# Kernel tuning notes

Hardware: AMD Instinct MI355X
Metric: run time of the kernel (lower is better)

Reference implementation:

```python
import jax, jax.numpy as jnp
import numpy as np

EPS_DEFAULT = 1.1920928955078125e-07  # torch fp32 finfo eps used when eps=None


def rms_norm(x, ndims, weight=None, eps=EPS_DEFAULT):
    # normalize over the last `ndims` dims, matching F.rms_norm semantics
    axes = tuple(range(x.ndim - ndims, x.ndim))
    ms = jnp.mean(jnp.square(x), axis=axes, keepdims=True)
    out = x * jax.lax.rsqrt(ms + eps)
    if weight is not None:
        out = out * weight  # weight broadcasts over trailing dims
    return out


def setup_inputs() -> dict:
    key = jax.random.key(0)
    ks = jax.random.split(key, 9)
    B, S = 32, 512
    return {
        "x": jax.random.normal(ks[0], (B, S, 12, 24), dtype=jnp.float32),
        "y": jax.random.normal(ks[1], (B, S, 12, 16), dtype=jnp.float32),
        "z": jax.random.normal(ks[2], (B, S, 12, 16, 24), dtype=jnp.float32),
        "w0": jax.random.uniform(ks[3], (24,), dtype=jnp.float32),
        "w1": jax.random.uniform(ks[4], (12, 16), dtype=jnp.float32),
        "w2": jax.random.uniform(ks[5], (24,), dtype=jnp.float32),
        "w3": jax.random.uniform(ks[6], (24,), dtype=jnp.float32),
        "w4": jax.random.uniform(ks[7], (12, 16), dtype=jnp.float32),
        "w5": jax.random.uniform(ks[8], (24,), dtype=jnp.float32),
    }


def reference(x, y, z, w0, w1, w2, w3, w4, w5):
    # x branch: norm over (24,), then (12,24), then (24,)
    x = rms_norm(x, 1, w0)
    x = rms_norm(x, 2, None)
    x = rms_norm(x, 1, w3)
    # y branch: norm over (16,) eps=1e-3, then (12,16) twice
    y = rms_norm(y, 1, None, eps=0.001)
    y = rms_norm(y, 2, w1)
    y = rms_norm(y, 2, w4)
    # z branch: norm over (24,), then (12,16,24) eps=1e-2, then (24,)
    z = rms_norm(z, 1, w2)
    z = rms_norm(z, 3, None, eps=0.01)
    z = rms_norm(z, 1, w5)
    return (x, y, z)
```

## Files before the change

### kernel.cpp

```cpp
#include <hip/hip_runtime.h>

#define EPS_DEF 1.1920928955078125e-07f

typedef float f4 __attribute__((ext_vector_type(4)));


__launch_bounds__(192)
__global__ void fused_rms_kernel(const float* __restrict__ x,
                                 const float* __restrict__ y,
                                 const float* __restrict__ z,
                                 const float* __restrict__ w0,
                                 const float* __restrict__ w1,
                                 const float* __restrict__ w2,
                                 const float* __restrict__ w3,
                                 const float* __restrict__ w4,
                                 const float* __restrict__ w5,
                                 float* __restrict__ ox,
                                 float* __restrict__ oy,
                                 float* __restrict__ oz)
{
    __shared__ __align__(16) float2 part[1152];
    __shared__ __align__(16) float  xs[288];
    __shared__ __align__(16) float  ys[192];
    __shared__ float2 rw[192];
    __shared__ float2 rwx[12];
    __shared__ float  rwy[12];
    __shared__ __align__(16) float w0sqs[24], w03s[24];
    __shared__ __align__(16) float w1sqs[192], w14s[192];
    __shared__ float wpart[3][4];

    const int tid = threadIdx.x;
    const int bid = blockIdx.x;
    const int j6  = tid % 6;
    const int c4  = j6 * 4;
    const int r0  = tid / 6;

    float w2v[4], w5v[4];
    #pragma unroll
    for (int k = 0; k < 4; ++k) { w2v[k] = w2[c4 + k]; w5v[k] = w5[c4 + k]; }

    const f4* zp = (const f4*)(z + (size_t)bid * 4608);
    f4 zr[6];
    #pragma unroll
    for (int i = 0; i < 6; ++i) zr[i] = zp[tid + 192 * i];

    if (tid < 72) {
        ((f4*)xs)[tid] = ((const f4*)(x + (size_t)bid * 288))[tid];
    } else if (tid < 120) {
        int t = tid - 72;
        ((f4*)ys)[t] = ((const f4*)(y + (size_t)bid * 192))[t];
    } else if (tid < 144) {
        int q = tid - 120;
        float a0 = w0[q], a3 = w3[q];
        w0sqs[q] = a0 * a0; w03s[q] = a0 * a3;
    }
    {
        float a1 = w1[tid], a4 = w4[tid];
        w1sqs[tid] = a1 * a1;
        w14s[tid]  = a1 * a4;
    }

    #pragma unroll
    for (int i = 0; i < 6; ++i) {
        f4 q = zr[i];
        float s0 = q.x * q.x;
        s0 = fmaf(q.y, q.y, s0); s0 = fmaf(q.z, q.z, s0); s0 = fmaf(q.w, q.w, s0);
        float t0 = q.x * w2v[0], t1 = q.y * w2v[1], t2 = q.z * w2v[2], t3 = q.w * w2v[3];
        float sw = t0 * t0;
        sw = fmaf(t1, t1, sw); sw = fmaf(t2, t2, sw); sw = fmaf(t3, t3, sw);
        part[tid + 192 * i] = make_float2(s0, sw);
    }
    __syncthreads();

    float s0 = 0.f, swz = 0.f;
    {
        const f4* pr = (const f4*)&part[6 * tid];
        #pragma unroll
        for (int k = 0; k < 3; ++k) {
            f4 p = pr[k];
            s0  += p.x + p.z;
            swz += p.y + p.w;
        }
    }
    const float r1 = rsqrtf(s0 * (1.f / 24.f) + EPS_DEF);
    rw[tid] = make_float2(r1, swz);
    float p0 = r1 * r1 * swz, p1 = 0.f, p2 = 0.f, p3 = 0.f;

    if (tid < 12) {
        const float* row = &xs[tid * 24];
        float a0 = 0.f, aw = 0.f;
        #pragma unroll
        for (int j = 0; j < 24; ++j) {
            float v = row[j];
            a0 = fmaf(v, v, a0);
            aw = fmaf(v * v, w0sqs[j], aw);
        }
        float r1x = rsqrtf(a0 * (1.f / 24.f) + EPS_DEF);
        rwx[tid] = make_float2(r1x, aw);
        p1 = r1x * r1x * aw;
    } else if (tid < 24) {
        int i = tid - 12;
        const float* row = &ys[i * 16];
        const float* wq  = &w1sqs[i * 16];
        float a0 = 0.f, aw = 0.f;
        #pragma unroll
        for (int j = 0; j < 16; ++j) {
            float v = row[j];
            a0 = fmaf(v, v, a0);
            aw = fmaf(v * v, wq[j], aw);
        }
        float r1y = rsqrtf(a0 * (1.f / 16.f) + 1e-3f);
        rwy[i] = r1y;
        p2 = r1y * r1y * a0;
        p3 = r1y * r1y * aw;
    }

    #pragma unroll
    for (int d = 32; d; d >>= 1) {
        p0 += __shfl_down(p0, d, 64);
        p1 += __shfl_down(p1, d, 64);
        p2 += __shfl_down(p2, d, 64);
        p3 += __shfl_down(p3, d, 64);
    }
    if ((tid & 63) == 0) {
        int w = tid >> 6;
        wpart[w][0] = p0; wpart[w][1] = p1; wpart[w][2] = p2; wpart[w][3] = p3;
    }
    __syncthreads();

    const float Sz  = wpart[0][0] + wpart[1][0] + wpart[2][0];
    const float Sx  = wpart[0][1] + wpart[1][1] + wpart[2][1];
    const float Sy0 = wpart[0][2] + wpart[1][2] + wpart[2][2];
    const float Sy1 = wpart[0][3] + wpart[1][3] + wpart[2][3];

    const float cZ  = rsqrtf(Sz  * (1.f / 4608.f) + 0.01f);
    const float cX  = rsqrtf(Sx  * (1.f / 288.f)  + EPS_DEF);
    const float c2y = rsqrtf(Sy0 * (1.f / 192.f)  + EPS_DEF);
    const float c3y = rsqrtf(c2y * c2y * Sy1 * (1.f / 192.f) + EPS_DEF);
    const float cZsq = cZ * cZ;

    {
        float w25r[4];
        #pragma unroll
        for (int k = 0; k < 4; ++k) w25r[k] = w2v[k] * w5v[k];
        f4* ozp = (f4*)(oz + (size_t)bid * 4608);
        #pragma unroll
        for (int i = 0; i < 6; ++i) {
            float2 rr = rw[r0 + 32 * i];
            float r3 = rsqrtf(cZsq * rr.x * rr.x * rr.y * (1.f / 24.f) + EPS_DEF);
            float a  = rr.x * cZ * r3;
            f4 q = zr[i];
            q.x *= a * w25r[0];
            q.y *= a * w25r[1];
            q.z *= a * w25r[2];
            q.w *= a * w25r[3];
            __builtin_nontemporal_store(q, ozp + tid + 192 * i);
        }
    }

    if (tid < 72) {
        int row = tid / 6;
        float2 rr = rwx[row];
        float r3 = rsqrtf(cX * cX * rr.x * rr.x * rr.y * (1.f / 24.f) + EPS_DEF);
        float ax = rr.x * cX * r3;
        f4 q = ((const f4*)xs)[tid];
        f4 wf = ((const f4*)w03s)[tid % 6];
        q.x *= ax * wf.x;
        q.y *= ax * wf.y;
        q.z *= ax * wf.z;
        q.w *= ax * wf.w;
        __builtin_nontemporal_store(q, (f4*)(ox + (size_t)bid * 288) + tid);
    } else if (tid < 120) {
        int t = tid - 72;
        float ay = rwy[t / 4] * c2y * c3y;
        f4 q = ((const f4*)ys)[t];
        f4 wf = ((const f4*)w14s)[t];
        q.x *= ay * wf.x;
        q.y *= ay * wf.y;
        q.z *= ay * wf.z;
        q.w *= ay * wf.w;
        __builtin_nontemporal_store(q, (f4*)(oy + (size_t)bid * 192) + t);
    }
}

extern "C" void kernel_launch(void* const* d_in, const int* in_sizes, int n_in,
                              void* d_out, int out_size, void* d_ws, size_t ws_size,
                              hipStream_t stream) {
    const float* x  = (const float*)d_in[0];
    const float* y  = (const float*)d_in[1];
    const float* z  = (const float*)d_in[2];
    const float* w0 = (const float*)d_in[3];
    const float* w1 = (const float*)d_in[4];
    const float* w2 = (const float*)d_in[5];
    const float* w3 = (const float*)d_in[6];
    const float* w4 = (const float*)d_in[7];
    const float* w5 = (const float*)d_in[8];

    float* out = (float*)d_out;
    const size_t NX = (size_t)32 * 512 * 12 * 24;
    const size_t NY = (size_t)32 * 512 * 12 * 16;
    float* ox = out;
    float* oy = out + NX;
    float* oz = out + NX + NY;

    const int nblk = 32 * 512;
    hipLaunchKernelGGL(fused_rms_kernel, dim3(nblk), dim3(192), 0, stream,
                       x, y, z, w0, w1, w2, w3, w4, w5, ox, oy, oz);
}
```

Baseline: 123.3 us.

## Process two sequence slots per block and use nontemporal loads

Each 192-thread block now handles two (b,s) slots instead of one, halving the grid and loading both slots' z/x/y data up front so more memory loads are in flight per thread. The weight-product setup and barriers are amortized over two slots, and the wave reductions carry eight partial sums instead of four. Input loads are switched to nontemporal. The cost is double the register and LDS footprint per block, which may reduce occupancy.

Result: no change. 122.2 us (-0.9%).

```diff
diff --git a/kernel.cpp b/kernel.cpp
--- a/kernel.cpp
+++ b/kernel.cpp
@@ -19,18 +19,18 @@
                                  float* __restrict__ oy,
                                  float* __restrict__ oz)
 {
-    __shared__ __align__(16) float2 part[1152];
-    __shared__ __align__(16) float  xs[288];
-    __shared__ __align__(16) float  ys[192];
-    __shared__ float2 rw[192];
-    __shared__ float2 rwx[12];
-    __shared__ float  rwy[12];
+    __shared__ __align__(16) float2 part[2][1152];
+    __shared__ __align__(16) float  xs[2][288];
+    __shared__ __align__(16) float  ys[2][192];
+    __shared__ float2 rw[2][192];
+    __shared__ float2 rwx[2][12];
+    __shared__ float  rwy[2][12];
     __shared__ __align__(16) float w0sqs[24], w03s[24];
     __shared__ __align__(16) float w1sqs[192], w14s[192];
-    __shared__ float wpart[3][4];
+    __shared__ float wpart[3][8];
 
     const int tid = threadIdx.x;
-    const int bid = blockIdx.x;
+    const size_t slA = (size_t)blockIdx.x * 2;
     const int j6  = tid % 6;
     const int c4  = j6 * 4;
     const int r0  = tid / 6;
@@ -39,16 +39,26 @@
     #pragma unroll
     for (int k = 0; k < 4; ++k) { w2v[k] = w2[c4 + k]; w5v[k] = w5[c4 + k]; }
 
-    const f4* zp = (const f4*)(z + (size_t)bid * 4608);
-    f4 zr[6];
-    #pragma unroll
-    for (int i = 0; i < 6; ++i) zr[i] = zp[tid + 192 * i];
+    f4 zr[2][6];
+    #pragma unroll
+    for (int s = 0; s < 2; ++s) {
+        const f4* zp = (const f4*)(z + (slA + s) * 4608);
+        #pragma unroll
+        for (int i = 0; i < 6; ++i)
+            zr[s][i] = __builtin_nontemporal_load(zp + tid + 192 * i);
+    }
 
     if (tid < 72) {
-        ((f4*)xs)[tid] = ((const f4*)(x + (size_t)bid * 288))[tid];
+        #pragma unroll
+        for (int s = 0; s < 2; ++s)
+            ((f4*)xs[s])[tid] =
+                __builtin_nontemporal_load((const f4*)(x + (slA + s) * 288) + tid);
     } else if (tid < 120) {
         int t = tid - 72;
-        ((f4*)ys)[t] = ((const f4*)(y + (size_t)bid * 192))[t];
+        #pragma unroll
+        for (int s = 0; s < 2; ++s)
+            ((f4*)ys[s])[t] =
+                __builtin_nontemporal_load((const f4*)(y + (slA + s) * 192) + t);
     } else if (tid < 144) {
         int q = tid - 120;
         float a0 = w0[q], a3 = w3[q];
@@ -61,125 +71,140 @@
     }
 
     #pragma unroll
-    for (int i = 0; i < 6; ++i) {
-        f4 q = zr[i];
-        float s0 = q.x * q.x;
-        s0 = fmaf(q.y, q.y, s0); s0 = fmaf(q.z, q.z, s0); s0 = fmaf(q.w, q.w, s0);
-        float t0 = q.x * w2v[0], t1 = q.y * w2v[1], t2 = q.z * w2v[2], t3 = q.w * w2v[3];
-        float sw = t0 * t0;
-        sw = fmaf(t1, t1, sw); sw = fmaf(t2, t2, sw); sw = fmaf(t3, t3, sw);
-        part[tid + 192 * i] = make_float2(s0, sw);
+    for (int s = 0; s < 2; ++s) {
+        #pragma unroll
+        for (int i = 0; i < 6; ++i) {
+            f4 q = zr[s][i];
+            float a0 = q.x * q.x;
+            a0 = fmaf(q.y, q.y, a0); a0 = fmaf(q.z, q.z, a0); a0 = fmaf(q.w, q.w, a0);
+            float t0 = q.x * w2v[0], t1 = q.y * w2v[1], t2 = q.z * w2v[2], t3 = q.w * w2v[3];
+            float aw = t0 * t0;
+            aw = fmaf(t1, t1, aw); aw = fmaf(t2, t2, aw); aw = fmaf(t3, t3, aw);
+            part[s][tid + 192 * i] = make_float2(a0, aw);
+        }
     }
     __syncthreads();
 
-    float s0 = 0.f, swz = 0.f;
-    {
-        const f4* pr = (const f4*)&part[6 * tid];
+    float p[8];
+    #pragma unroll
+    for (int q = 0; q < 8; ++q) p[q] = 0.f;
+
+    #pragma unroll
+    for (int s = 0; s < 2; ++s) {
+        float a0 = 0.f, aw = 0.f;
+        const f4* pr = (const f4*)&part[s][6 * tid];
         #pragma unroll
         for (int k = 0; k < 3; ++k) {
-            f4 p = pr[k];
-            s0  += p.x + p.z;
-            swz += p.y + p.w;
-        }
-    }
-    const float r1 = rsqrtf(s0 * (1.f / 24.f) + EPS_DEF);
-    rw[tid] = make_float2(r1, swz);
-    float p0 = r1 * r1 * swz, p1 = 0.f, p2 = 0.f, p3 = 0.f;
+            f4 pp = pr[k];
+            a0 += pp.x + pp.z;
+            aw += pp.y + pp.w;
+        }
+        float r1 = rsqrtf(a0 * (1.f / 24.f) + EPS_DEF);
+        rw[s][tid] = make_float2(r1, aw);
+        p[4 * s + 0] = r1 * r1 * aw;
+    }
 
     if (tid < 12) {
-        const float* row = &xs[tid * 24];
-        float a0 = 0.f, aw = 0.f;
-        #pragma unroll
-        for (int j = 0; j < 24; ++j) {
-            float v = row[j];
-            a0 = fmaf(v, v, a0);
-            aw = fmaf(v * v, w0sqs[j], aw);
-        }
-        float r1x = rsqrtf(a0 * (1.f / 24.f) + EPS_DEF);
-        rwx[tid] = make_float2(r1x, aw);
-        p1 = r1x * r1x * aw;
+        #pragma unroll
+        for (int s = 0; s < 2; ++s) {
+            const float* row = &xs[s][tid * 24];
+            float a0 = 0.f, aw = 0.f;
+            #pragma unroll
+            for (int j = 0; j < 24; ++j) {
+                float v = row[j];
+                a0 = fmaf(v, v, a0);
+                aw = fmaf(v * v, w0sqs[j], aw);
+            }
+            float r1x = rsqrtf(a0 * (1.f / 24.f) + EPS_DEF);
+            rwx[s][tid] = make_float2(r1x, aw);
+            p[4 * s + 1] = r1x * r1x * aw;
+        }
     } else if (tid < 24) {
         int i = tid - 12;
-        const float* row = &ys[i * 16];
-        const float* wq  = &w1sqs[i * 16];
-        float a0 = 0.f, aw = 0.f;
-        #pragma unroll
-        for (int j = 0; j < 16; ++j) {
-            float v = row[j];
-            a0 = fmaf(v, v, a0);
-            aw = fmaf(v * v, wq[j], aw);
-        }
-        float r1y = rsqrtf(a0 * (1.f / 16.f) + 1e-3f);
-        rwy[i] = r1y;
-        p2 = r1y * r1y * a0;
-        p3 = r1y * r1y * aw;
+        #pragma unroll
+        for (int s = 0; s < 2; ++s) {
+            const float* row = &ys[s][i * 16];
+            const float* wq  = &w1sqs[i * 16];
+            float a0 = 0.f, aw = 0.f;
+            #pragma unroll
+            for (int j = 0; j < 16; ++j) {
+                float v = row[j];
+                a0 = fmaf(v, v, a0);
+                aw = fmaf(v * v, wq[j], aw);
+            }
+            float r1y = rsqrtf(a0 * (1.f / 16.f) + 1e-3f);
+            rwy[s][i] = r1y;
+            p[4 * s + 2] = r1y * r1y * a0;
+            p[4 * s + 3] = r1y * r1y * aw;
+        }
     }
 
     #pragma unroll
     for (int d = 32; d; d >>= 1) {
-        p0 += __shfl_down(p0, d, 64);
-        p1 += __shfl_down(p1, d, 64);
-        p2 += __shfl_down(p2, d, 64);
-        p3 += __shfl_down(p3, d, 64);
+        #pragma unroll
+        for (int q = 0; q < 8; ++q) p[q] += __shfl_down(p[q], d, 64);
     }
     if ((tid & 63) == 0) {
         int w = tid >> 6;
-        wpart[w][0] = p0; wpart[w][1] = p1; wpart[w][2] = p2; wpart[w][3] = p3;
+        #pragma unroll
+        for (int q = 0; q < 8; ++q) wpart[w][q] = p[q];
     }
     __syncthreads();
 
-    const float Sz  = wpart[0][0] + wpart[1][0] + wpart[2][0];
-    const float Sx  = wpart[0][1] + wpart[1][1] + wpart[2][1];
-    const float Sy0 = wpart[0][2] + wpart[1][2] + wpart[2][2];
-    const float Sy1 = wpart[0][3] + wpart[1][3] + wpart[2][3];
-
-    const float cZ  = rsqrtf(Sz  * (1.f / 4608.f) + 0.01f);
-    const float cX  = rsqrtf(Sx  * (1.f / 288.f)  + EPS_DEF);
-    const float c2y = rsqrtf(Sy0 * (1.f / 192.f)  + EPS_DEF);
-    const float c3y = rsqrtf(c2y * c2y * Sy1 * (1.f / 192.f) + EPS_DEF);
-    const float cZsq = cZ * cZ;
-
-    {
-        float w25r[4];
-        #pragma unroll
-        for (int k = 0; k < 4; ++k) w25r[k] = w2v[k] * w5v[k];
-        f4* ozp = (f4*)(oz + (size_t)bid * 4608);
+    float w25r[4];
+    #pragma unroll
+    for (int k = 0; k < 4; ++k) w25r[k] = w2v[k] * w5v[k];
+
+    #pragma unroll
+    for (int s = 0; s < 2; ++s) {
+        const float Sz  = wpart[0][4*s+0] + wpart[1][4*s+0] + wpart[2][4*s+0];
+        const float Sx  = wpart[0][4*s+1] + wpart[1][4*s+1] + wpart[2][4*s+1];
+        const float Sy0 = wpart[0][4*s+2] + wpart[1][4*s+2] + wpart[2][4*s+2];
+        const float Sy1 = wpart[0][4*s+3] + wpart[1][4*s+3] + wpart[2][4*s+3];
+
+        const float cZ  = rsqrtf(Sz  * (1.f / 4608.f) + 0.01f);
+        const float cX  = rsqrtf(Sx  * (1.f / 288.f)  + EPS_DEF);
+        const float c2y = rsqrtf(Sy0 * (1.f / 192.f)  + EPS_DEF);
+        const float c3y = rsqrtf(c2y * c2y * Sy1 * (1.f / 192.f) + EPS_DEF);
+        const float cZsq = cZ * cZ;
+
+        f4* ozp = (f4*)(oz + (slA + s) * 4608);
         #pragma unroll
         for (int i = 0; i < 6; ++i) {
-            float2 rr = rw[r0 + 32 * i];
+            float2 rr = rw[s][r0 + 32 * i];
             float r3 = rsqrtf(cZsq * rr.x * rr.x * rr.y * (1.f / 24.f) + EPS_DEF);
             float a  = rr.x * cZ * r3;
-            f4 q = zr[i];
+            f4 q = zr[s][i];
             q.x *= a * w25r[0];
             q.y *= a * w25r[1];
             q.z *= a * w25r[2];
             q.w *= a * w25r[3];
             __builtin_nontemporal_store(q, ozp + tid + 192 * i);
         }
-    }
-
-    if (tid < 72) {
-        int row = tid / 6;
-        float2 rr = rwx[row];
-        float r3 = rsqrtf(cX * cX * rr.x * rr.x * rr.y * (1.f / 24.f) + EPS_DEF);
-        float ax = rr.x * cX * r3;
-        f4 q = ((const f4*)xs)[tid];
-        f4 wf = ((const f4*)w03s)[tid % 6];
-        q.x *= ax * wf.x;
-        q.y *= ax * wf.y;
-        q.z *= ax * wf.z;
-        q.w *= ax * wf.w;
-        __builtin_nontemporal_store(q, (f4*)(ox + (size_t)bid * 288) + tid);
-    } else if (tid < 120) {
-        int t = tid - 72;
-        float ay = rwy[t / 4] * c2y * c3y;
-        f4 q = ((const f4*)ys)[t];
-        f4 wf = ((const f4*)w14s)[t];
-        q.x *= ay * wf.x;
-        q.y *= ay * wf.y;
-        q.z *= ay * wf.z;
-        q.w *= ay * wf.w;
-        __builtin_nontemporal_store(q, (f4*)(oy + (size_t)bid * 192) + t);
+
+        if (tid < 72) {
+            int row = tid / 6;
+            float2 rr = rwx[s][row];
+            float r3 = rsqrtf(cX * cX * rr.x * rr.x * rr.y * (1.f / 24.f) + EPS_DEF);
+            float ax = rr.x * cX * r3;
+            f4 q = ((const f4*)xs[s])[tid];
+            f4 wf = ((const f4*)w03s)[tid % 6];
+            q.x *= ax * wf.x;
+            q.y *= ax * wf.y;
+            q.z *= ax * wf.z;
+            q.w *= ax * wf.w;
+            __builtin_nontemporal_store(q, (f4*)(ox + (slA + s) * 288) + tid);
+        } else if (tid < 120) {
+            int t = tid - 72;
+            float ay = rwy[s][t / 4] * c2y * c3y;
+            f4 q = ((const f4*)ys[s])[t];
+            f4 wf = ((const f4*)w14s)[t];
+            q.x *= ay * wf.x;
+            q.y *= ay * wf.y;
+            q.z *= ay * wf.z;
+            q.w *= ay * wf.w;
+            __builtin_nontemporal_store(q, (f4*)(oy + (slA + s) * 192) + t);
+        }
     }
 }
 
@@ -203,7 +228,7 @@
     float* oy = out + NX;
     float* oz = out + NX + NY;
 
-    const int nblk = 32 * 512;
+    const int nblk = 32 * 512 / 2;
     hipLaunchKernelGGL(fused_rms_kernel, dim3(nblk), dim3(192), 0, stream,
                        x, y, z, w0, w1, w2, w3, w4, w5, ox, oy, oz);
 }
```
